# Performance work log

Hardware: AMD Instinct MI355X
Metric: run time of the kernel (lower is better)

Reference implementation:

```python
import jax, jax.numpy as jnp
import numpy as np

MAX_SPAN_LEN = 20
LN_EPS = 1e-12


def _layer_norm(x, g, b):
    mu = jnp.mean(x, axis=-1, keepdims=True)
    var = jnp.mean(jnp.square(x - mu), axis=-1, keepdims=True)
    return (x - mu) * jax.lax.rsqrt(var + LN_EPS) * g + b


def _gelu(x):
    return jax.nn.gelu(x, approximate=False)  # exact BERT gelu


def setup_inputs() -> dict:
    key = jax.random.key(0)
    ks = jax.random.split(key, 8)
    bs, seq_len, dim = 8, 512, 768
    num_pairs, pe, emb, vocab = 32, 200, 128, 30522
    d_in = 2 * dim + pe
    s = lambda n: 1.0 / np.sqrt(n)
    return {
        "hidden_states": jax.random.normal(ks[0], (bs, seq_len, dim), jnp.float32),
        "pairs": jax.random.randint(ks[1], (bs, num_pairs, 2), 0, seq_len, jnp.int64 if jax.config.jax_enable_x64 else jnp.int32),
        "pos_emb": jax.random.normal(ks[2], (MAX_SPAN_LEN, pe), jnp.float32) * 0.02,
        "W1": jax.random.normal(ks[3], (d_in, dim), jnp.float32) * s(d_in),
        "b1": jnp.zeros((dim,), jnp.float32),
        "g1": jnp.ones((dim,), jnp.float32),
        "be1": jnp.zeros((dim,), jnp.float32),
        "W2": jax.random.normal(ks[4], (dim, dim), jnp.float32) * s(dim),
        "b2": jnp.zeros((dim,), jnp.float32),
        "g2": jnp.ones((dim,), jnp.float32),
        "be2": jnp.zeros((dim,), jnp.float32),
        "Wp": jax.random.normal(ks[5], (dim, emb), jnp.float32) * s(dim),
        "bp": jnp.zeros((emb,), jnp.float32),
        "Wdec": jax.random.normal(ks[6], (vocab, emb), jnp.float32) * 0.02,
    }


def reference(hidden_states, pairs, pos_emb, W1, b1, g1, be1, W2, b2, g2, be2, Wp, bp, Wdec):
    bs, num_pairs, _ = pairs.shape
    dim = hidden_states.shape[-1]
    # gather span endpoint hidden states: [bs, num_pairs, dim]
    left = jnp.take_along_axis(hidden_states, pairs[:, :, 0:1], axis=1) if False else None
    lh = jnp.take_along_axis(hidden_states, pairs[:, :, 0][..., None].astype(jnp.int32) * jnp.ones((1, 1, dim), jnp.int32), axis=1)
    rh = jnp.take_along_axis(hidden_states, pairs[:, :, 1][..., None].astype(jnp.int32) * jnp.ones((1, 1, dim), jnp.int32), axis=1)
    lh = lh.reshape(bs * num_pairs, 1, dim)
    rh = rh.reshape(bs * num_pairs, 1, dim)
    # broadcast over span positions and concat with position embeddings: [B*P, L, 2*dim+pe]
    B = bs * num_pairs
    L = MAX_SPAN_LEN
    x = jnp.concatenate([
        jnp.broadcast_to(lh, (B, L, dim)),
        jnp.broadcast_to(rh, (B, L, dim)),
        jnp.broadcast_to(pos_emb[None], (B, L, pos_emb.shape[-1])),
    ], axis=-1)
    h = _layer_norm(_gelu(x @ W1 + b1), g1, be1)
    h = _layer_norm(_gelu(h @ W2 + b2), g2, be2)
    h = h @ Wp + bp  # embeddings_project (embedding_size != hidden_size)
    return jnp.einsum("ble,ve->blv", h, Wdec)  # decoder, no bias
```

## Files before the change

### kernel.cpp

```cpp
#include <hip/hip_runtime.h>
#include <math.h>

#define DIM    768
#define PE     200
#define LSPAN  20
#define NPAIRS 256
#define ROWS   5120
#define EMB    128
#define VOCAB  30522

typedef __attribute__((ext_vector_type(8))) short short8;
typedef __attribute__((ext_vector_type(4))) float floatx4;

__device__ inline unsigned short f2bf(float f) {
    union { float f; unsigned int u; } v; v.f = f;
    unsigned int r = v.u + 0x7fffu + ((v.u >> 16) & 1u);
    return (unsigned short)(r >> 16);
}
__device__ inline float gelu_exact(float x) {
    return 0.5f * x * (1.0f + erff(x * 0.70710678118654752f));
}

__global__ void k_f32_to_bf16_vec4(const float* __restrict__ src, unsigned short* __restrict__ dst, int n4) {
    int i = blockIdx.x * blockDim.x + threadIdx.x;
    if (i >= n4) return;
    float4 v = ((const float4*)src)[i];
    ushort4 o;
    o.x = f2bf(v.x); o.y = f2bf(v.y); o.z = f2bf(v.z); o.w = f2bf(v.w);
    ((ushort4*)dst)[i] = o;
}

__global__ __launch_bounds__(256) void k_transpose_bf16t(const float* __restrict__ src,
                                                         unsigned short* __restrict__ dst,
                                                         int R, int C) {
    __shared__ float ls[64][65];
    int r0 = blockIdx.x * 64, c0 = blockIdx.y * 64;
    int tid = threadIdx.x;
#pragma unroll
    for (int i = 0; i < 16; ++i) {
        int idx = tid + i * 256;
        int lr = idx >> 6, lc = idx & 63;
        ls[lr][lc] = src[(size_t)(r0 + lr) * C + c0 + lc];
    }
    __syncthreads();
#pragma unroll
    for (int i = 0; i < 16; ++i) {
        int idx = tid + i * 256;
        int oc = idx >> 6, orr = idx & 63;
        dst[(size_t)(c0 + oc) * R + r0 + orr] = f2bf(ls[orr][oc]);
    }
}

__global__ __launch_bounds__(256) void k_posW(const float* __restrict__ pos_emb, const float* __restrict__ W1,
                                              const float* __restrict__ b1, float* __restrict__ posW) {
    __shared__ float pe_s[PE];
    int l = blockIdx.x, tid = threadIdx.x;
    if (tid < PE) pe_s[tid] = pos_emb[l * PE + tid];
    __syncthreads();
    for (int jj = 0; jj < 3; ++jj) {
        int j = jj * 256 + tid;
        float acc = b1[j];
        for (int k = 0; k < PE; ++k)
            acc += pe_s[k] * W1[(size_t)(2 * DIM + k) * DIM + j];
        posW[l * DIM + j] = acc;
    }
}

__global__ __launch_bounds__(256) void k_pairW(const float* __restrict__ hs, const int* __restrict__ pairs,
                                               const float* __restrict__ W1, float* __restrict__ pairW) {
    __shared__ float lh_s[4][DIM];
    __shared__ float rh_s[4][DIM];
    int tid = threadIdx.x;
    int jc = blockIdx.x;
    int g  = blockIdx.y;
    for (int p4 = 0; p4 < 4; ++p4) {
        int p = g * 4 + p4;
        int batch = p >> 5;
        int li = pairs[p * 2 + 0];
        int ri = pairs[p * 2 + 1];
        const float* lrow = hs + ((size_t)batch * 512 + li) * DIM;
        const float* rrow = hs + ((size_t)batch * 512 + ri) * DIM;
        for (int jj = 0; jj < 3; ++jj) {
            lh_s[p4][jj * 256 + tid] = lrow[jj * 256 + tid];
            rh_s[p4][jj * 256 + tid] = rrow[jj * 256 + tid];
        }
    }
    __syncthreads();
    int j = jc * 256 + tid;
    float a0 = 0.f, a1 = 0.f, a2 = 0.f, a3 = 0.f;
    for (int k = 0; k < DIM; ++k) {
        float w1a = W1[(size_t)k * DIM + j];
        float w1b = W1[(size_t)(DIM + k) * DIM + j];
        a0 += lh_s[0][k] * w1a + rh_s[0][k] * w1b;
        a1 += lh_s[1][k] * w1a + rh_s[1][k] * w1b;
        a2 += lh_s[2][k] * w1a + rh_s[2][k] * w1b;
        a3 += lh_s[3][k] * w1a + rh_s[3][k] * w1b;
    }
    pairW[(size_t)(g * 4 + 0) * DIM + j] = a0;
    pairW[(size_t)(g * 4 + 1) * DIM + j] = a1;
    pairW[(size_t)(g * 4 + 2) * DIM + j] = a2;
    pairW[(size_t)(g * 4 + 3) * DIM + j] = a3;
}

__global__ __launch_bounds__(256) void k_h1(const float* __restrict__ pairW, const float* __restrict__ posW,
                                            const float* __restrict__ g1, const float* __restrict__ be1,
                                            unsigned short* __restrict__ h1) {
    __shared__ float xs[DIM];
    __shared__ float red[10];
    int row = blockIdx.x, tid = threadIdx.x;
    int p = row / LSPAN, l = row % LSPAN;
    float s = 0.f, s2 = 0.f;
    for (int jj = 0; jj < 3; ++jj) {
        int j = jj * 256 + tid;
        float v = pairW[(size_t)p * DIM + j] + posW[l * DIM + j];
        float gv = gelu_exact(v);
        xs[j] = gv;
        s += gv; s2 += gv * gv;
    }
    for (int off = 32; off > 0; off >>= 1) { s += __shfl_down(s, off); s2 += __shfl_down(s2, off); }
    int w = tid >> 6, lane = tid & 63;
    if (lane == 0) { red[w] = s; red[4 + w] = s2; }
    __syncthreads();
    if (tid == 0) {
        float a = red[0] + red[1] + red[2] + red[3];
        float b = red[4] + red[5] + red[6] + red[7];
        float mu = a / DIM;
        float var = fmaxf(b / DIM - mu * mu, 0.f);
        red[8] = mu; red[9] = rsqrtf(var + 1e-12f);
    }
    __syncthreads();
    float mu = red[8], rstd = red[9];
    for (int jj = 0; jj < 3; ++jj) {
        int j = jj * 256 + tid;
        h1[(size_t)row * DIM + j] = f2bf((xs[j] - mu) * rstd * g1[j] + be1[j]);
    }
}

__global__ __launch_bounds__(256) void k_ln(const float* __restrict__ in, const float* __restrict__ gamma,
                                            const float* __restrict__ beta, unsigned short* __restrict__ out) {
    __shared__ float xs[DIM];
    __shared__ float red[10];
    int row = blockIdx.x, tid = threadIdx.x;
    float s = 0.f, s2 = 0.f;
    for (int jj = 0; jj < 3; ++jj) {
        int j = jj * 256 + tid;
        float v = in[(size_t)row * DIM + j];
        xs[j] = v;
        s += v; s2 += v * v;
    }
    for (int off = 32; off > 0; off >>= 1) { s += __shfl_down(s, off); s2 += __shfl_down(s2, off); }
    int w = tid >> 6, lane = tid & 63;
    if (lane == 0) { red[w] = s; red[4 + w] = s2; }
    __syncthreads();
    if (tid == 0) {
        float a = red[0] + red[1] + red[2] + red[3];
        float b = red[4] + red[5] + red[6] + red[7];
        float mu = a / DIM;
        float var = fmaxf(b / DIM - mu * mu, 0.f);
        red[8] = mu; red[9] = rsqrtf(var + 1e-12f);
    }
    __syncthreads();
    float mu = red[8], rstd = red[9];
    for (int jj = 0; jj < 3; ++jj) {
        int j = jj * 256 + tid;
        out[(size_t)row * DIM + j] = f2bf((xs[j] - mu) * rstd * gamma[j] + beta[j]);
    }
}

template <int EPI>
__global__ __launch_bounds__(256) void gemm_bt(const unsigned short* __restrict__ A,
                                               const unsigned short* __restrict__ B,
                                               const float* __restrict__ bias, void* __restrict__ Cout,
                                               int M, int N, int K, int ldc) {
    const int LDT = 136;
    __shared__ unsigned short As[64 * LDT];
    __shared__ unsigned short Bs[64 * LDT];
    int tid = threadIdx.x;
    int bx = ((blockIdx.x & 7) * (gridDim.x >> 3)) + (blockIdx.x >> 3);
    int m0 = bx * 64;
    int n0 = blockIdx.y * 64;
    int w = tid >> 6, lane = tid & 63;
    int quad = lane >> 4, r16 = lane & 15;
    int wm = (w >> 1) * 32, wn = (w & 1) * 32;

    floatx4 acc[2][2] = {};

    for (int k0 = 0; k0 < K; k0 += 128) {
#pragma unroll
        for (int i = 0; i < 4; ++i) {
            int c = tid + i * 256;
            int row = c >> 4;
            int kc = (c & 15) * 8;
            uint4 v = *(const uint4*)(&A[(size_t)(m0 + row) * K + k0 + kc]);
            *(uint4*)(&As[row * LDT + kc]) = v;
        }
#pragma unroll
        for (int i = 0; i < 4; ++i) {
            int c = tid + i * 256;
            int row = c >> 4;
            int kc = (c & 15) * 8;
            uint4 v = make_uint4(0u, 0u, 0u, 0u);
            if (n0 + row < N)
                v = *(const uint4*)(&B[(size_t)(n0 + row) * K + k0 + kc]);
            *(uint4*)(&Bs[row * LDT + kc]) = v;
        }
        __syncthreads();
#pragma unroll
        for (int kk = 0; kk < 4; ++kk) {
            short8 a0 = *(const short8*)(&As[(wm + 0 * 16 + r16) * LDT + kk * 32 + quad * 8]);
            short8 a1 = *(const short8*)(&As[(wm + 1 * 16 + r16) * LDT + kk * 32 + quad * 8]);
            short8 b0 = *(const short8*)(&Bs[(wn + 0 * 16 + r16) * LDT + kk * 32 + quad * 8]);
            short8 b1 = *(const short8*)(&Bs[(wn + 1 * 16 + r16) * LDT + kk * 32 + quad * 8]);
            acc[0][0] = __builtin_amdgcn_mfma_f32_16x16x32_bf16(a0, b0, acc[0][0], 0, 0, 0);
            acc[0][1] = __builtin_amdgcn_mfma_f32_16x16x32_bf16(a0, b1, acc[0][1], 0, 0, 0);
            acc[1][0] = __builtin_amdgcn_mfma_f32_16x16x32_bf16(a1, b0, acc[1][0], 0, 0, 0);
            acc[1][1] = __builtin_amdgcn_mfma_f32_16x16x32_bf16(a1, b1, acc[1][1], 0, 0, 0);
        }
        __syncthreads();
    }

#pragma unroll
    for (int mt = 0; mt < 2; ++mt)
#pragma unroll
        for (int nt = 0; nt < 2; ++nt)
#pragma unroll
            for (int r = 0; r < 4; ++r) {
                int row = m0 + wm + mt * 16 + quad * 4 + r;
                int col = n0 + wn + nt * 16 + r16;
                if (col < N) {
                    float v = acc[mt][nt][r];
                    if (EPI == 1) {
                        v = gelu_exact(v + bias[col]);
                        ((float*)Cout)[(size_t)row * ldc + col] = v;
                    } else if (EPI == 2) {
                        v += bias[col];
                        ((unsigned short*)Cout)[(size_t)row * ldc + col] = f2bf(v);
                    } else {
                        ((float*)Cout)[(size_t)row * ldc + col] = v;
                    }
                }
            }
}

#define DEC_NB  239
#define DEC_MB  80
#define DEC_NPX 30

__global__ __launch_bounds__(256) void gemm_dec(const unsigned short* __restrict__ A,
                                                const unsigned short* __restrict__ B,
                                                float* __restrict__ C) {
    const int LDT = 136;
    __shared__ unsigned short As[64 * LDT];
    __shared__ unsigned short Bs[128 * LDT];
    int flat = blockIdx.x;
    int xcd = flat & 7;
    int j = flat >> 3;
    int m = j % DEC_MB;
    int npl = j / DEC_MB;
    int npanel = xcd * DEC_NPX + npl;
    if (npanel >= DEC_NB) return;
    int m0 = m * 64;
    int n0 = npanel * 128;
    int tid = threadIdx.x;
    int w = tid >> 6, lane = tid & 63;
    int quad = lane >> 4, r16 = lane & 15;
    int wm = (w >> 1) * 32, wn = (w & 1) * 64;

#pragma unroll
    for (int i = 0; i < 4; ++i) {
        int c = tid + i * 256;
        int row = c >> 4, kc = (c & 15) * 8;
        *(uint4*)(&As[row * LDT + kc]) = *(const uint4*)(&A[(size_t)(m0 + row) * 128 + kc]);
    }
#pragma unroll
    for (int i = 0; i < 8; ++i) {
        int c = tid + i * 256;
        int row = c >> 4, kc = (c & 15) * 8;
        int brow = n0 + row;
        if (brow >= VOCAB) brow = VOCAB - 1;
        *(uint4*)(&Bs[row * LDT + kc]) = *(const uint4*)(&B[(size_t)brow * 128 + kc]);
    }
    __syncthreads();

    floatx4 acc[2][4] = {};
#pragma unroll
    for (int kk = 0; kk < 4; ++kk) {
        short8 a0 = *(const short8*)(&As[(wm + 0 * 16 + r16) * LDT + kk * 32 + quad * 8]);
        short8 a1 = *(const short8*)(&As[(wm + 1 * 16 + r16) * LDT + kk * 32 + quad * 8]);
        short8 b0 = *(const short8*)(&Bs[(wn + 0 * 16 + r16) * LDT + kk * 32 + quad * 8]);
        short8 b1 = *(const short8*)(&Bs[(wn + 1 * 16 + r16) * LDT + kk * 32 + quad * 8]);
        short8 b2 = *(const short8*)(&Bs[(wn + 2 * 16 + r16) * LDT + kk * 32 + quad * 8]);
        short8 b3 = *(const short8*)(&Bs[(wn + 3 * 16 + r16) * LDT + kk * 32 + quad * 8]);
        acc[0][0] = __builtin_amdgcn_mfma_f32_16x16x32_bf16(a0, b0, acc[0][0], 0, 0, 0);
        acc[0][1] = __builtin_amdgcn_mfma_f32_16x16x32_bf16(a0, b1, acc[0][1], 0, 0, 0);
        acc[0][2] = __builtin_amdgcn_mfma_f32_16x16x32_bf16(a0, b2, acc[0][2], 0, 0, 0);
        acc[0][3] = __builtin_amdgcn_mfma_f32_16x16x32_bf16(a0, b3, acc[0][3], 0, 0, 0);
        acc[1][0] = __builtin_amdgcn_mfma_f32_16x16x32_bf16(a1, b0, acc[1][0], 0, 0, 0);
        acc[1][1] = __builtin_amdgcn_mfma_f32_16x16x32_bf16(a1, b1, acc[1][1], 0, 0, 0);
        acc[1][2] = __builtin_amdgcn_mfma_f32_16x16x32_bf16(a1, b2, acc[1][2], 0, 0, 0);
        acc[1][3] = __builtin_amdgcn_mfma_f32_16x16x32_bf16(a1, b3, acc[1][3], 0, 0, 0);
    }

#pragma unroll
    for (int mt = 0; mt < 2; ++mt)
#pragma unroll
        for (int nt = 0; nt < 4; ++nt)
#pragma unroll
            for (int r = 0; r < 4; ++r) {
                int row = m0 + wm + mt * 16 + quad * 4 + r;
                int col = n0 + wn + nt * 16 + r16;
                if (col < VOCAB)
                    C[(size_t)row * VOCAB + col] = acc[mt][nt][r];
            }
}

extern "C" void kernel_launch(void* const* d_in, const int* in_sizes, int n_in,
                              void* d_out, int out_size, void* d_ws, size_t ws_size,
                              hipStream_t stream) {
    const float* hs      = (const float*)d_in[0];
    const int*   pairs   = (const int*)d_in[1];
    const float* pos_emb = (const float*)d_in[2];
    const float* W1      = (const float*)d_in[3];
    const float* b1      = (const float*)d_in[4];
    const float* g1      = (const float*)d_in[5];
    const float* be1     = (const float*)d_in[6];
    const float* W2      = (const float*)d_in[7];
    const float* b2      = (const float*)d_in[8];
    const float* g2      = (const float*)d_in[9];
    const float* be2     = (const float*)d_in[10];
    const float* Wp      = (const float*)d_in[11];
    const float* bp      = (const float*)d_in[12];
    const float* Wdec    = (const float*)d_in[13];
    float* out = (float*)d_out;

    char* ws = (char*)d_ws;
    float*          posW  = (float*)(ws + 0);
    float*          pairW = (float*)(ws + 61440);
    unsigned short* h1    = (unsigned short*)(ws + 847872);
    unsigned short* W2T   = (unsigned short*)(ws + 8712192);
    float*          y     = (float*)(ws + 9891840);
    unsigned short* h2    = (unsigned short*)(ws + 25620480);
    unsigned short* WpT   = (unsigned short*)(ws + 33484800);
    unsigned short* h3    = (unsigned short*)(ws + 33681408);
    unsigned short* WdecB = (unsigned short*)(ws + 34992128);

    int n4 = (VOCAB * EMB) / 4;
    k_f32_to_bf16_vec4<<<(n4 + 255) / 256, 256, 0, stream>>>(Wdec, WdecB, n4);
    k_transpose_bf16t<<<dim3(DIM / 64, DIM / 64), 256, 0, stream>>>(W2, W2T, DIM, DIM);
    k_transpose_bf16t<<<dim3(DIM / 64, EMB / 64), 256, 0, stream>>>(Wp, WpT, DIM, EMB);

    k_posW<<<LSPAN, 256, 0, stream>>>(pos_emb, W1, b1, posW);
    k_pairW<<<dim3(3, 64), 256, 0, stream>>>(hs, pairs, W1, pairW);
    k_h1<<<ROWS, 256, 0, stream>>>(pairW, posW, g1, be1, h1);

    gemm_bt<1><<<dim3(ROWS / 64, DIM / 64), 256, 0, stream>>>(h1, W2T, b2, y, ROWS, DIM, DIM, DIM);
    k_ln<<<ROWS, 256, 0, stream>>>(y, g2, be2, h2);

    gemm_bt<2><<<dim3(ROWS / 64, EMB / 64), 256, 0, stream>>>(h2, WpT, bp, h3, ROWS, EMB, DIM, EMB);

    gemm_dec<<<8 * DEC_NPX * DEC_MB, 256, 0, stream>>>(h3, WdecB, out);
}
```

Before: 970.5 us.

## Merge weight-prep kernels and reuse decoder B tile across multiple M tiles

```diff
diff --git a/kernel.cpp b/kernel.cpp
--- a/kernel.cpp
+++ b/kernel.cpp
@@ -21,40 +21,50 @@
     return 0.5f * x * (1.0f + erff(x * 0.70710678118654752f));
 }
 
-__global__ void k_f32_to_bf16_vec4(const float* __restrict__ src, unsigned short* __restrict__ dst, int n4) {
-    int i = blockIdx.x * blockDim.x + threadIdx.x;
-    if (i >= n4) return;
-    float4 v = ((const float4*)src)[i];
-    ushort4 o;
-    o.x = f2bf(v.x); o.y = f2bf(v.y); o.z = f2bf(v.z); o.w = f2bf(v.w);
-    ((ushort4*)dst)[i] = o;
-}
-
-__global__ __launch_bounds__(256) void k_transpose_bf16t(const float* __restrict__ src,
-                                                         unsigned short* __restrict__ dst,
-                                                         int R, int C) {
+#define PREP_CONV 3816
+#define PREP_T1   3960
+#define PREP_T2   3984
+#define PREP_TOT  4004
+
+__global__ __launch_bounds__(256) void k_prep(const float* __restrict__ Wdec, unsigned short* __restrict__ WdecB,
+                                              const float* __restrict__ W2, unsigned short* __restrict__ W2T,
+                                              const float* __restrict__ Wp, unsigned short* __restrict__ WpT,
+                                              const float* __restrict__ pos_emb, const float* __restrict__ W1,
+                                              const float* __restrict__ b1, float* __restrict__ posW) {
     __shared__ float ls[64][65];
-    int r0 = blockIdx.x * 64, c0 = blockIdx.y * 64;
-    int tid = threadIdx.x;
-#pragma unroll
-    for (int i = 0; i < 16; ++i) {
-        int idx = tid + i * 256;
-        int lr = idx >> 6, lc = idx & 63;
-        ls[lr][lc] = src[(size_t)(r0 + lr) * C + c0 + lc];
-    }
-    __syncthreads();
-#pragma unroll
-    for (int i = 0; i < 16; ++i) {
-        int idx = tid + i * 256;
-        int oc = idx >> 6, orr = idx & 63;
-        dst[(size_t)(c0 + oc) * R + r0 + orr] = f2bf(ls[orr][oc]);
-    }
-}
-
-__global__ __launch_bounds__(256) void k_posW(const float* __restrict__ pos_emb, const float* __restrict__ W1,
-                                              const float* __restrict__ b1, float* __restrict__ posW) {
-    __shared__ float pe_s[PE];
-    int l = blockIdx.x, tid = threadIdx.x;
+    int b = blockIdx.x, tid = threadIdx.x;
+    if (b < PREP_CONV) {
+        int i = b * 256 + tid;
+        if (i < (VOCAB * EMB) / 4) {
+            float4 v = ((const float4*)Wdec)[i];
+            ushort4 o;
+            o.x = f2bf(v.x); o.y = f2bf(v.y); o.z = f2bf(v.z); o.w = f2bf(v.w);
+            ((ushort4*)WdecB)[i] = o;
+        }
+        return;
+    }
+    if (b < PREP_T2) {
+        const float* src; unsigned short* dst; int C, R, tr, tc;
+        if (b < PREP_T1) { int bb = b - PREP_CONV; src = W2; dst = W2T; R = DIM; C = DIM; tr = bb / 12; tc = bb % 12; }
+        else             { int bb = b - PREP_T1;   src = Wp; dst = WpT; R = DIM; C = EMB; tr = bb / 2;  tc = bb % 2;  }
+        int r0 = tr * 64, c0 = tc * 64;
+#pragma unroll
+        for (int i = 0; i < 16; ++i) {
+            int idx = tid + i * 256;
+            int lr = idx >> 6, lc = idx & 63;
+            ls[lr][lc] = src[(size_t)(r0 + lr) * C + c0 + lc];
+        }
+        __syncthreads();
+#pragma unroll
+        for (int i = 0; i < 16; ++i) {
+            int idx = tid + i * 256;
+            int oc = idx >> 6, orr = idx & 63;
+            dst[(size_t)(c0 + oc) * R + r0 + orr] = f2bf(ls[orr][oc]);
+        }
+        return;
+    }
+    int l = b - PREP_T2;
+    float* pe_s = &ls[0][0];
     if (tid < PE) pe_s[tid] = pos_emb[l * PE + tid];
     __syncthreads();
     for (int jj = 0; jj < 3; ++jj) {
@@ -242,9 +252,10 @@
             }
 }
 
-#define DEC_NB  239
-#define DEC_MB  80
-#define DEC_NPX 30
+#define DEC_NB   239
+#define DEC_NPX  30
+#define DEC_MPER 8
+#define DEC_MGRP 10
 
 __global__ __launch_bounds__(256) void gemm_dec(const unsigned short* __restrict__ A,
                                                 const unsigned short* __restrict__ B,
@@ -255,23 +266,16 @@
     int flat = blockIdx.x;
     int xcd = flat & 7;
     int j = flat >> 3;
-    int m = j % DEC_MB;
-    int npl = j / DEC_MB;
+    int npl = j % DEC_NPX;
+    int mg  = j / DEC_NPX;
     int npanel = xcd * DEC_NPX + npl;
     if (npanel >= DEC_NB) return;
-    int m0 = m * 64;
     int n0 = npanel * 128;
     int tid = threadIdx.x;
     int w = tid >> 6, lane = tid & 63;
     int quad = lane >> 4, r16 = lane & 15;
     int wm = (w >> 1) * 32, wn = (w & 1) * 64;
 
-#pragma unroll
-    for (int i = 0; i < 4; ++i) {
-        int c = tid + i * 256;
-        int row = c >> 4, kc = (c & 15) * 8;
-        *(uint4*)(&As[row * LDT + kc]) = *(const uint4*)(&A[(size_t)(m0 + row) * 128 + kc]);
-    }
 #pragma unroll
     for (int i = 0; i < 8; ++i) {
         int c = tid + i * 256;
@@ -280,38 +284,49 @@
         if (brow >= VOCAB) brow = VOCAB - 1;
         *(uint4*)(&Bs[row * LDT + kc]) = *(const uint4*)(&B[(size_t)brow * 128 + kc]);
     }
-    __syncthreads();
-
-    floatx4 acc[2][4] = {};
-#pragma unroll
-    for (int kk = 0; kk < 4; ++kk) {
-        short8 a0 = *(const short8*)(&As[(wm + 0 * 16 + r16) * LDT + kk * 32 + quad * 8]);
-        short8 a1 = *(const short8*)(&As[(wm + 1 * 16 + r16) * LDT + kk * 32 + quad * 8]);
-        short8 b0 = *(const short8*)(&Bs[(wn + 0 * 16 + r16) * LDT + kk * 32 + quad * 8]);
-        short8 b1 = *(const short8*)(&Bs[(wn + 1 * 16 + r16) * LDT + kk * 32 + quad * 8]);
-        short8 b2 = *(const short8*)(&Bs[(wn + 2 * 16 + r16) * LDT + kk * 32 + quad * 8]);
-        short8 b3 = *(const short8*)(&Bs[(wn + 3 * 16 + r16) * LDT + kk * 32 + quad * 8]);
-        acc[0][0] = __builtin_amdgcn_mfma_f32_16x16x32_bf16(a0, b0, acc[0][0], 0, 0, 0);
-        acc[0][1] = __builtin_amdgcn_mfma_f32_16x16x32_bf16(a0, b1, acc[0][1], 0, 0, 0);
-        acc[0][2] = __builtin_amdgcn_mfma_f32_16x16x32_bf16(a0, b2, acc[0][2], 0, 0, 0);
-        acc[0][3] = __builtin_amdgcn_mfma_f32_16x16x32_bf16(a0, b3, acc[0][3], 0, 0, 0);
-        acc[1][0] = __builtin_amdgcn_mfma_f32_16x16x32_bf16(a1, b0, acc[1][0], 0, 0, 0);
-        acc[1][1] = __builtin_amdgcn_mfma_f32_16x16x32_bf16(a1, b1, acc[1][1], 0, 0, 0);
-        acc[1][2] = __builtin_amdgcn_mfma_f32_16x16x32_bf16(a1, b2, acc[1][2], 0, 0, 0);
-        acc[1][3] = __builtin_amdgcn_mfma_f32_16x16x32_bf16(a1, b3, acc[1][3], 0, 0, 0);
-    }
-
-#pragma unroll
-    for (int mt = 0; mt < 2; ++mt)
-#pragma unroll
-        for (int nt = 0; nt < 4; ++nt)
-#pragma unroll
-            for (int r = 0; r < 4; ++r) {
-                int row = m0 + wm + mt * 16 + quad * 4 + r;
-                int col = n0 + wn + nt * 16 + r16;
-                if (col < VOCAB)
-                    C[(size_t)row * VOCAB + col] = acc[mt][nt][r];
-            }
+
+    for (int t = 0; t < DEC_MPER; ++t) {
+        int m0 = (mg * DEC_MPER + t) * 64;
+#pragma unroll
+        for (int i = 0; i < 4; ++i) {
+            int c = tid + i * 256;
+            int row = c >> 4, kc = (c & 15) * 8;
+            *(uint4*)(&As[row * LDT + kc]) = *(const uint4*)(&A[(size_t)(m0 + row) * 128 + kc]);
+        }
+        __syncthreads();
+
+        floatx4 acc[2][4] = {};
+#pragma unroll
+        for (int kk = 0; kk < 4; ++kk) {
+            short8 a0 = *(const short8*)(&As[(wm + 0 * 16 + r16) * LDT + kk * 32 + quad * 8]);
+            short8 a1 = *(const short8*)(&As[(wm + 1 * 16 + r16) * LDT + kk * 32 + quad * 8]);
+            short8 b0 = *(const short8*)(&Bs[(wn + 0 * 16 + r16) * LDT + kk * 32 + quad * 8]);
+            short8 b1 = *(const short8*)(&Bs[(wn + 1 * 16 + r16) * LDT + kk * 32 + quad * 8]);
+            short8 b2 = *(const short8*)(&Bs[(wn + 2 * 16 + r16) * LDT + kk * 32 + quad * 8]);
+            short8 b3 = *(const short8*)(&Bs[(wn + 3 * 16 + r16) * LDT + kk * 32 + quad * 8]);
+            acc[0][0] = __builtin_amdgcn_mfma_f32_16x16x32_bf16(a0, b0, acc[0][0], 0, 0, 0);
+            acc[0][1] = __builtin_amdgcn_mfma_f32_16x16x32_bf16(a0, b1, acc[0][1], 0, 0, 0);
+            acc[0][2] = __builtin_amdgcn_mfma_f32_16x16x32_bf16(a0, b2, acc[0][2], 0, 0, 0);
+            acc[0][3] = __builtin_amdgcn_mfma_f32_16x16x32_bf16(a0, b3, acc[0][3], 0, 0, 0);
+            acc[1][0] = __builtin_amdgcn_mfma_f32_16x16x32_bf16(a1, b0, acc[1][0], 0, 0, 0);
+            acc[1][1] = __builtin_amdgcn_mfma_f32_16x16x32_bf16(a1, b1, acc[1][1], 0, 0, 0);
+            acc[1][2] = __builtin_amdgcn_mfma_f32_16x16x32_bf16(a1, b2, acc[1][2], 0, 0, 0);
+            acc[1][3] = __builtin_amdgcn_mfma_f32_16x16x32_bf16(a1, b3, acc[1][3], 0, 0, 0);
+        }
+        __syncthreads();
+
+#pragma unroll
+        for (int mt = 0; mt < 2; ++mt)
+#pragma unroll
+            for (int nt = 0; nt < 4; ++nt)
+#pragma unroll
+                for (int r = 0; r < 4; ++r) {
+                    int row = m0 + wm + mt * 16 + quad * 4 + r;
+                    int col = n0 + wn + nt * 16 + r16;
+                    if (col < VOCAB)
+                        C[(size_t)row * VOCAB + col] = acc[mt][nt][r];
+                }
+    }
 }
 
 extern "C" void kernel_launch(void* const* d_in, const int* in_sizes, int n_in,
@@ -344,12 +359,8 @@
     unsigned short* h3    = (unsigned short*)(ws + 33681408);
     unsigned short* WdecB = (unsigned short*)(ws + 34992128);
 
-    int n4 = (VOCAB * EMB) / 4;
-    k_f32_to_bf16_vec4<<<(n4 + 255) / 256, 256, 0, stream>>>(Wdec, WdecB, n4);
-    k_transpose_bf16t<<<dim3(DIM / 64, DIM / 64), 256, 0, stream>>>(W2, W2T, DIM, DIM);
-    k_transpose_bf16t<<<dim3(DIM / 64, EMB / 64), 256, 0, stream>>>(Wp, WpT, DIM, EMB);
-
-    k_posW<<<LSPAN, 256, 0, stream>>>(pos_emb, W1, b1, posW);
+    k_prep<<<PREP_TOT, 256, 0, stream>>>(Wdec, WdecB, W2, W2T, Wp, WpT, pos_emb, W1, b1, posW);
+
     k_pairW<<<dim3(3, 64), 256, 0, stream>>>(hs, pairs, W1, pairW);
     k_h1<<<ROWS, 256, 0, stream>>>(pairW, posW, g1, be1, h1);
 
@@ -358,5 +369,5 @@
 
     gemm_bt<2><<<dim3(ROWS / 64, EMB / 64), 256, 0, stream>>>(h2, WpT, bp, h3, ROWS, EMB, DIM, EMB);
 
-    gemm_dec<<<8 * DEC_NPX * DEC_MB, 256, 0, stream>>>(h3, WdecB, out);
-}
+    gemm_dec<<<8 * DEC_NPX * DEC_MGRP, 256, 0, stream>>>(h3, WdecB, out);
+}
```

New measurement: 915.7 us. 1.06x faster.
